# Kernel optimization log

Hardware: AMD Instinct MI355X
Metric: run time of the kernel (lower is better)

The kernel has to match this reference:

```python
import jax, jax.numpy as jnp
import numpy as np

B, N, E = 128, 300, 300        # batch, nodes (max_length), edges per sample
DIN, DH, DOUT = 768, 256, 256  # input feat, gcn hidden, gcn output
R = 26                         # NUM_DEP_TYPES
NHEADS, HDIM = 8, DH // 8


def setup_inputs() -> dict:
    key = jax.random.key(0)
    ks = jax.random.split(key, 12)
    s = lambda d: 1.0 / np.sqrt(d)
    return {
        "node_features": jax.random.normal(ks[0], (B, N, DIN), jnp.float32),
        "src": jax.random.randint(ks[1], (B, E), 0, N, jnp.int32),
        "dst": jax.random.randint(ks[2], (B, E), 0, N, jnp.int32),
        "etype": jax.random.randint(ks[3], (B, E), 0, R, jnp.int32),
        "W_rel": jax.random.normal(ks[4], (R, DIN, DH), jnp.float32) * s(DIN),
        "W_loop": jax.random.normal(ks[5], (DIN, DH), jnp.float32) * s(DIN),
        "b_rel": jnp.zeros((DH,), jnp.float32),
        "in_proj_w": jax.random.normal(ks[6], (3 * DH, DH), jnp.float32) * s(DH),
        "in_proj_b": jnp.zeros((3 * DH,), jnp.float32),
        "out_proj_w": jax.random.normal(ks[7], (DH, DH), jnp.float32) * s(DH),
        "out_proj_b": jnp.zeros((DH,), jnp.float32),
        "mlp_w": jax.random.normal(ks[8], (DOUT, DH), jnp.float32) * s(DH),
        "mlp_b": jnp.zeros((DOUT,), jnp.float32),
    }


def reference(node_features, src, dst, etype, W_rel, W_loop, b_rel,
              in_proj_w, in_proj_b, out_proj_w, out_proj_b, mlp_w, mlp_b):
    # ---- RelGraphConv (regularizer=None, self_loop=True, sum aggregation) ----
    # gather source-node features per edge: [B, E, DIN]
    h_src = jnp.take_along_axis(node_features, src[..., None].astype(jnp.int32), axis=1)
    # per-relation masked matmul: msg[b,e] = h_src[b,e] @ W_rel[etype[b,e]]
    msg = jnp.zeros((B, E, DH), node_features.dtype)
    for r in range(R):  # fixed small relation set
        mask = (etype == r)[..., None]
        msg = msg + jnp.einsum('bei,io->beo', jnp.where(mask, h_src, 0.0), W_rel[r])
    # scatter-add messages to destination nodes
    b_idx = jnp.arange(B)[:, None]
    agg = jnp.zeros((B, N, DH), node_features.dtype).at[b_idx, dst].add(msg)
    h = agg + jnp.einsum('bni,io->bno', node_features, W_loop) + b_rel  # [B, N, DH]

    # ---- MultiheadAttention (self-attn over nodes, eval mode) ----
    qkv = jnp.einsum('bnd,ed->bne', h, in_proj_w) + in_proj_b
    q, k, v = jnp.split(qkv, 3, axis=-1)
    q = q.reshape(B, N, NHEADS, HDIM)
    k = k.reshape(B, N, NHEADS, HDIM)
    v = v.reshape(B, N, NHEADS, HDIM)
    scores = jnp.einsum('bqhd,bkhd->bhqk', q, k) / np.sqrt(HDIM)
    attn = jax.nn.softmax(scores, axis=-1)
    ctx = jnp.einsum('bhqk,bkhd->bqhd', attn, v).reshape(B, N, DH)
    attn_out = jnp.einsum('bnd,ed->bne', ctx, out_proj_w) + out_proj_b

    # ---- mean-pool over nodes + MLP ----
    pooled = jnp.mean(attn_out, axis=1)  # [B, DH]
    return pooled @ mlp_w.T + mlp_b      # [B, DOUT]
```

## Files before the change

kernel.cpp:

```cpp
#include <hip/hip_runtime.h>
#include <hip/hip_bf16.h>
#include <cstdint>
#include <cstddef>

#define BB 128
#define NN 300
#define EE 300
#define DIN 768
#define DH 256
#define NREL 26
#define NHEADS 8
#define HDIM 32
#define MTOT (BB*NN)
#define NEDGE (BB*EE)
#define NHB 150

typedef __attribute__((ext_vector_type(8))) short bf16x8;
typedef __attribute__((ext_vector_type(4))) float f32x4;
typedef unsigned short u16;
union BU { uint4 u; bf16x8 v; };

__device__ __forceinline__ unsigned int packbf2(float a, float b) {
    unsigned int ua = __float_as_uint(a);
    unsigned int ub = __float_as_uint(b);
    ua = (ua + 0x7FFFu + ((ua >> 16) & 1u)) >> 16;
    ub = (ub + 0x7FFFu + ((ub >> 16) & 1u)) & 0xFFFF0000u;
    return ua | ub;
}
__device__ __forceinline__ u16 packbf1(float a) {
    unsigned int ua = __float_as_uint(a);
    return (u16)((ua + 0x7FFFu + ((ua >> 16) & 1u)) >> 16);
}
__device__ __forceinline__ unsigned cvtpk(float a, float b) {
    union { __hip_bfloat162 h; unsigned u; } cv;
    cv.h = __float22bfloat162_rn(make_float2(a, b));
    return cv.u;
}

__global__ __launch_bounds__(256) void b_hist(const int* __restrict__ etype,
                                              int* __restrict__ blockhist) {
    __shared__ int hist[NREL];
    const int tid = threadIdx.x;
    if (tid < NREL) hist[tid] = 0;
    __syncthreads();
    atomicAdd(&hist[etype[blockIdx.x * 256 + tid]], 1);
    __syncthreads();
    if (tid < NREL) blockhist[blockIdx.x * NREL + tid] = hist[tid];
}

__global__ __launch_bounds__(64) void b_scan(const int* __restrict__ blockhist,
                                             int* __restrict__ blockbase,
                                             int* __restrict__ cnt, int* __restrict__ off) {
    __shared__ int tot[NREL];
    const int r = threadIdx.x;
    if (r < NREL) {
        int run = 0;
        for (int b = 0; b < NHB; ++b) {
            blockbase[b * NREL + r] = run;
            run += blockhist[b * NREL + r];
        }
        tot[r] = run;
        cnt[r] = run;
    }
    __syncthreads();
    __shared__ int offs[NREL + 1];
    if (r == 0) {
        int acc = 0;
        for (int q = 0; q < NREL; ++q) { offs[q] = acc; off[q] = acc; acc += tot[q]; }
        offs[NREL] = acc; off[NREL] = acc;
    }
    __syncthreads();
    if (r < NREL) {
        int o = offs[r];
        for (int b = 0; b < NHB; ++b) blockbase[b * NREL + r] += o;
    }
}

__global__ __launch_bounds__(256) void b_scatter(const int* __restrict__ etype,
                                                 const int* __restrict__ blockbase,
                                                 int* __restrict__ list) {
    __shared__ int wavehist[4][NREL];
    __shared__ int waveoff[4][NREL];
    const int tid = threadIdx.x;
    const int w = tid >> 6, l = tid & 63;
    const int i = blockIdx.x * 256 + tid;
    const int r = etype[i];
    unsigned long long mymask = 0ull;
    #pragma unroll
    for (int q = 0; q < NREL; ++q) {
        unsigned long long m = __ballot(r == q);
        if (l == 0) wavehist[w][q] = __popcll(m);
        if (r == q) mymask = m;
    }
    const int myrank = __popcll(mymask & ((1ull << l) - 1ull));
    __syncthreads();
    if (tid < NREL) {
        int acc = 0;
        #pragma unroll
        for (int ww = 0; ww < 4; ++ww) { waveoff[ww][tid] = acc; acc += wavehist[ww][tid]; }
    }
    __syncthreads();
    list[blockbase[blockIdx.x * NREL + r] + waveoff[w][r] + myrank] = i;
}

__global__ __launch_bounds__(128) void z_tail(uint4* __restrict__ vg4) {
    const int p = blockIdx.x;
    const int tid = threadIdx.x;
    const int f = (tid < 64) ? 9 : 19;
    const int t = tid & 63;
    vg4[(size_t)(p * 20 + f) * 64 + t] = make_uint4(0u, 0u, 0u, 0u);
}

__global__ __launch_bounds__(256) void c_cast8(const float4* __restrict__ in,
                                               uint4* __restrict__ out, int n8) {
    int i = blockIdx.x * 256 + threadIdx.x;
    if (i < n8) {
        float4 f0 = in[2*i], f1 = in[2*i+1];
        uint4 o;
        o.x = packbf2(f0.x, f0.y); o.y = packbf2(f0.z, f0.w);
        o.z = packbf2(f1.x, f1.y); o.w = packbf2(f1.z, f1.w);
        out[i] = o;
    }
}

__global__ __launch_bounds__(256) void c_cast_w(
    const float* __restrict__ wrel, const float* __restrict__ wl, const float* __restrict__ wq,
    uint4* __restrict__ wrb, uint4* __restrict__ wlb, uint4* __restrict__ wqb) {
    int t = blockIdx.x * 256 + threadIdx.x;
    int l = t & 63, fid = t >> 6;
    if (fid < NREL*24*16) {
        int r = fid / 384, rem = fid - r * 384;
        int kf = rem >> 4, nt = rem & 15;
        int k0 = 32*kf + 8*(l >> 4), n = 16*nt + (l & 15);
        const float* p = wrel + ((size_t)r*768 + k0) * 256 + n;
        uint4 o;
        o.x = packbf2(p[0], p[256]); o.y = packbf2(p[512], p[768]);
        o.z = packbf2(p[1024], p[1280]); o.w = packbf2(p[1536], p[1792]);
        wrb[t] = o;
    } else if (fid < NREL*24*16 + 384) {
        int f2 = fid - NREL*24*16;
        int kf = f2 >> 4, nt = f2 & 15;
        int k0 = 32*kf + 8*(l >> 4), n = 16*nt + (l & 15);
        const float* p = wl + (size_t)k0 * 256 + n;
        uint4 o;
        o.x = packbf2(p[0], p[256]); o.y = packbf2(p[512], p[768]);
        o.z = packbf2(p[1024], p[1280]); o.w = packbf2(p[1536], p[1792]);
        wlb[f2*64 + l] = o;
    } else {
        int f2 = fid - NREL*24*16 - 384;
        int kf = f2 / 48, nt = f2 % 48;
        int e = 16*nt + (l & 15), d0 = 32*kf + 8*(l >> 4);
        const float4* p = (const float4*)(wq + (size_t)e * 256 + d0);
        float4 f0 = p[0], f1 = p[1];
        uint4 o;
        o.x = packbf2(f0.x, f0.y); o.y = packbf2(f0.z, f0.w);
        o.z = packbf2(f1.x, f1.y); o.w = packbf2(f1.z, f1.w);
        wqb[f2*64 + l] = o;
    }
}

__global__ __launch_bounds__(256) void k1m(
    const uint4* __restrict__ xb, const uint4* __restrict__ wlb,
    const float* __restrict__ brel, float* __restrict__ h) {
    __shared__ uint4 As[512];
    const int tid = threadIdx.x;
    const int m0 = blockIdx.x * 64;
    const int nb = blockIdx.y;
    const int w = tid >> 6, l = tid & 63;
    const int g = l >> 4, q = l & 15;
    int cA[2];
    #pragma unroll
    for (int p = 0; p < 2; ++p) {
        int s = tid + p * 256;
        int fi = s >> 6, l2 = s & 63;
        int kf = fi >> 2, mt = fi & 3;
        int row = m0 + 16*mt + (l2 & 15);
        cA[p] = row * 96 + 4*kf + (l2 >> 4);
    }
    f32x4 acc[4][2];
    #pragma unroll
    for (int a = 0; a < 4; ++a)
        #pragma unroll
        for (int n = 0; n < 2; ++n) acc[a][n] = (f32x4){0.f,0.f,0.f,0.f};

    for (int step = 0; step < 12; ++step) {
        uint4 a0 = xb[cA[0] + step*8];
        uint4 a1 = xb[cA[1] + step*8];
        BU Bf[2][2];
        #pragma unroll
        for (int kf = 0; kf < 2; ++kf)
            #pragma unroll
            for (int nt = 0; nt < 2; ++nt)
                Bf[kf][nt].u = wlb[((step*2 + kf)*16 + nb*8 + w*2 + nt)*64 + l];
        __syncthreads();
        As[tid] = a0; As[tid + 256] = a1;
        __syncthreads();
        #pragma unroll
        for (int kf = 0; kf < 2; ++kf) {
            BU Af[4];
            #pragma unroll
            for (int mt = 0; mt < 4; ++mt) Af[mt].u = As[(kf*4 + mt)*64 + l];
            #pragma unroll
            for (int mt = 0; mt < 4; ++mt)
                #pragma unroll
                for (int nt = 0; nt < 2; ++nt)
                    acc[mt][nt] = __builtin_amdgcn_mfma_f32_16x16x32_bf16(Af[mt].v, Bf[kf][nt].v, acc[mt][nt], 0, 0, 0);
        }
    }
    #pragma unroll
    for (int nt = 0; nt < 2; ++nt) {
        int col = nb*128 + w*32 + nt*16 + q;
        float bias = brel[col];
        #pragma unroll
        for (int mt = 0; mt < 4; ++mt)
            #pragma unroll
            for (int i = 0; i < 4; ++i)
                h[(size_t)(m0 + 16*mt + 4*g + i)*256 + col] = acc[mt][nt][i] + bias;
    }
}

__global__ __launch_bounds__(256) void k2m(
    const uint4* __restrict__ xb, const uint4* __restrict__ wrb,
    const int* __restrict__ src, const int* __restrict__ dst,
    const int* __restrict__ cnt, const int* __restrict__ off,
    const int* __restrict__ list, float* __restrict__ h) {
    __shared__ uint4 As[512];
    __shared__ int arow_s[64];
    __shared__ int drow_s[64];
    const int r = blockIdx.y;
    const int c_total = cnt[r];
    const int t0 = blockIdx.x * 64;
    if (t0 >= c_total) return;
    const int nb = blockIdx.z;
    const int tid = threadIdx.x;
    if (tid < 64) {
        int e = t0 + tid;
        int ar = 0, dr = -1;
        if (e < c_total) {
            int eid = list[off[r] + e];
            int b = eid / EE;
            ar = b * NN + src[eid];
            dr = b * NN + dst[eid];
        }
        arow_s[tid] = ar; drow_s[tid] = dr;
    }
    __syncthreads();
    const int w = tid >> 6, l = tid & 63;
    const int g = l >> 4, q = l & 15;
    int cA[2];
    #pragma unroll
    for (int p = 0; p < 2; ++p) {
        int s = tid + p * 256;
        int fi = s >> 6, l2 = s & 63;
        int kf = fi >> 2, mt = fi & 3;
        int row = arow_s[16*mt + (l2 & 15)];
        cA[p] = row * 96 + 4*kf + (l2 >> 4);
    }
    const uint4* wb = wrb + (size_t)r * 24*16*64;
    f32x4 acc[4][2];
    #pragma unroll
    for (int a = 0; a < 4; ++a)
        #pragma unroll
        for (int n = 0; n < 2; ++n) acc[a][n] = (f32x4){0.f,0.f,0.f,0.f};

    for (int step = 0; step < 12; ++step) {
        uint4 a0 = xb[cA[0] + step*8];
        uint4 a1 = xb[cA[1] + step*8];
        BU Bf[2][2];
        #pragma unroll
        for (int kf = 0; kf < 2; ++kf)
            #pragma unroll
            for (int nt = 0; nt < 2; ++nt)
                Bf[kf][nt].u = wb[((step*2 + kf)*16 + nb*8 + w*2 + nt)*64 + l];
        __syncthreads();
        As[tid] = a0; As[tid + 256] = a1;
        __syncthreads();
        #pragma unroll
        for (int kf = 0; kf < 2; ++kf) {
            BU Af[4];
            #pragma unroll
            for (int mt = 0; mt < 4; ++mt) Af[mt].u = As[(kf*4 + mt)*64 + l];
            #pragma unroll
            for (int mt = 0; mt < 4; ++mt)
                #pragma unroll
                for (int nt = 0; nt < 2; ++nt)
                    acc[mt][nt] = __builtin_amdgcn_mfma_f32_16x16x32_bf16(Af[mt].v, Bf[kf][nt].v, acc[mt][nt], 0, 0, 0);
        }
    }
    #pragma unroll
    for (int mt = 0; mt < 4; ++mt)
        #pragma unroll
        for (int i = 0; i < 4; ++i) {
            int dr = drow_s[16*mt + 4*g + i];
            if (dr >= 0) {
                #pragma unroll
                for (int nt = 0; nt < 2; ++nt)
                    atomicAdd(&h[(size_t)dr*256 + nb*128 + w*32 + nt*16 + q], acc[mt][nt][i]);
            }
        }
}

__global__ __launch_bounds__(256) void k3m(
    const uint4* __restrict__ hb, const uint4* __restrict__ wqb,
    const float* __restrict__ bq,
    u16* __restrict__ qg, u16* __restrict__ kg, u16* __restrict__ vg) {
    __shared__ uint4 As[512];
    const int tid = threadIdx.x;
    const int m0 = blockIdx.x * 64;
    const int nb = blockIdx.y;
    const int w = tid >> 6, l = tid & 63;
    const int g = l >> 4, q = l & 15;
    int cA[2];
    #pragma unroll
    for (int p = 0; p < 2; ++p) {
        int s = tid + p * 256;
        int fi = s >> 6, l2 = s & 63;
        int kf = fi >> 2, mt = fi & 3;
        int row = m0 + 16*mt + (l2 & 15);
        cA[p] = row * 32 + 4*kf + (l2 >> 4);
    }
    f32x4 acc[4][2];
    #pragma unroll
    for (int a = 0; a < 4; ++a)
        #pragma unroll
        for (int n = 0; n < 2; ++n) acc[a][n] = (f32x4){0.f,0.f,0.f,0.f};

    for (int step = 0; step < 4; ++step) {
        uint4 a0 = hb[cA[0] + step*8];
        uint4 a1 = hb[cA[1] + step*8];
        BU Bf[2][2];
        #pragma unroll
        for (int kf = 0; kf < 2; ++kf)
            #pragma unroll
            for (int nt = 0; nt < 2; ++nt)
                Bf[kf][nt].u = wqb[((step*2 + kf)*48 + nb*8 + w*2 + nt)*64 + l];
        __syncthreads();
        As[tid] = a0; As[tid + 256] = a1;
        __syncthreads();
        #pragma unroll
        for (int kf = 0; kf < 2; ++kf) {
            BU Af[4];
            #pragma unroll
            for (int mt = 0; mt < 4; ++mt) Af[mt].u = As[(kf*4 + mt)*64 + l];
            #pragma unroll
            for (int mt = 0; mt < 4; ++mt)
                #pragma unroll
                for (int nt = 0; nt < 2; ++nt)
                    acc[mt][nt] = __builtin_amdgcn_mfma_f32_16x16x32_bf16(Af[mt].v, Bf[kf][nt].v, acc[mt][nt], 0, 0, 0);
        }
    }
    #pragma unroll
    for (int nt = 0; nt < 2; ++nt) {
        int e = nb*128 + w*32 + nt*16 + q;
        float bias = bq[e];
        int region = e >> 8;
        int hh = (e & 255) >> 5;
        int d  = e & 31;
        u16* outb = (region == 0) ? qg : (region == 1) ? kg : vg;
        #pragma unroll
        for (int mt = 0; mt < 4; ++mt) {
            #pragma unroll
            for (int i = 0; i < 4; ++i) {
                int j = m0 + 16*mt + 4*g + i;
                int b_ = j / 300;
                int jn = j - b_ * 300;
                u16 val = packbf1(acc[mt][nt][i] + bias);
                size_t byte;
                if (region < 2) {
                    int word = ((b_*8 + hh)*19 + (jn >> 4))*64 + 16*(d >> 3) + (jn & 15);
                    byte = (size_t)word*16 + (size_t)(d & 7)*2;
                } else {
                    int word = ((b_*8 + hh)*20 + (d >> 4)*10 + (jn >> 5))*64 + 16*((jn >> 3) & 3) + (d & 15);
                    byte = (size_t)word*16 + (size_t)(jn & 7)*2;
                }
                *(u16*)((char*)outb + byte) = val;
            }
        }
    }
}

__global__ __launch_bounds__(256) void k4_attn(
    const uint4* __restrict__ qg, const uint4* __restrict__ kg,
    const uint4* __restrict__ vg, float* __restrict__ pooled) {
    __shared__ uint4 kf_s[19*64];
    __shared__ uint4 vt_s[20*64];
    __shared__ __align__(16) u16 pbuf[4][2560];
    __shared__ float pool_lds[4][32];
    const int bh = blockIdx.x;
    const int tid = threadIdx.x;
    for (int s = tid; s < 19*64; s += 256) kf_s[s] = kg[(size_t)bh*19*64 + s];
    for (int s = tid; s < 20*64; s += 256) vt_s[s] = vg[(size_t)bh*20*64 + s];
    __syncthreads();

    const int w = tid >> 6, l = tid & 63;
    const int g = l >> 4, q = l & 15;
    char* pwbase = (char*)pbuf[w] + 256*(g >> 1) + 16*q + 8*(g & 1);
    const uint4* prd = (const uint4*)pbuf[w];

    const float c1 = 0.17677669529663687f * 1.4426950408889634f;
    float pool[8] = {0.f,0.f,0.f,0.f,0.f,0.f,0.f,0.f};

    for (int qt = w; qt < 19; qt += 4) {
        const int qrow = qt * 16 + q;
        BU uq; uq.u = qg[(size_t)(bh*19 + qt)*64 + l];
        float lsum = 0.f;
        f32x4 ctx0 = {0.f,0.f,0.f,0.f}, ctx1 = {0.f,0.f,0.f,0.f};

        #pragma unroll
        for (int half = 0; half < 2; ++half) {
            #pragma unroll
            for (int jj = 0; jj < 10; ++jj) {
                const int jt = half*10 + jj;
                uint2 pk = make_uint2(0u, 0u);
                if (jt < 19) {
                    BU uk; uk.u = kf_s[jt*64 + l];
                    f32x4 z = {0.f,0.f,0.f,0.f};
                    f32x4 s4 = __builtin_amdgcn_mfma_f32_16x16x32_bf16(uk.v, uq.v, z, 0, 0, 0);
                    float p0 = exp2f(s4[0]*c1);
                    float p1 = exp2f(s4[1]*c1);
                    float p2 = exp2f(s4[2]*c1);
                    float p3 = exp2f(s4[3]*c1);
                    if (jt == 18 && g == 3) { p0 = 0.f; p1 = 0.f; p2 = 0.f; p3 = 0.f; }
                    lsum += (p0 + p1) + (p2 + p3);
                    pk.x = cvtpk(p0, p1);
                    pk.y = cvtpk(p2, p3);
                }
                *(uint2*)(pwbase + 512*jj) = pk;
            }
            #pragma unroll
            for (int cc = 0; cc < 5; ++cc) {
                const int cg = half*5 + cc;
                BU up;  up.u  = prd[cc*64 + l];
                BU uv0; uv0.u = vt_s[cg*64 + l];
                BU uv1; uv1.u = vt_s[(10 + cg)*64 + l];
                ctx0 = __builtin_amdgcn_mfma_f32_16x16x32_bf16(uv0.v, up.v, ctx0, 0, 0, 0);
                ctx1 = __builtin_amdgcn_mfma_f32_16x16x32_bf16(uv1.v, up.v, ctx1, 0, 0, 0);
            }
        }
        lsum += __shfl_xor(lsum, 16);
        lsum += __shfl_xor(lsum, 32);
        if (qrow < NN) {
            float inv = 1.0f / lsum;
            pool[0] += ctx0[0] * inv; pool[1] += ctx0[1] * inv;
            pool[2] += ctx0[2] * inv; pool[3] += ctx0[3] * inv;
            pool[4] += ctx1[0] * inv; pool[5] += ctx1[1] * inv;
            pool[6] += ctx1[2] * inv; pool[7] += ctx1[3] * inv;
        }
    }

    #pragma unroll
    for (int i = 0; i < 8; ++i) {
        float v = pool[i];
        v += __shfl_xor(v, 1); v += __shfl_xor(v, 2);
        v += __shfl_xor(v, 4); v += __shfl_xor(v, 8);
        pool[i] = v;
    }
    if (q == 0) {
        #pragma unroll
        for (int dt = 0; dt < 2; ++dt)
            #pragma unroll
            for (int i = 0; i < 4; ++i)
                pool_lds[w][dt * 16 + 4 * g + i] = pool[dt * 4 + i];
    }
    __syncthreads();
    if (tid < 32) {
        int b = bh >> 3, hh = bh & 7;
        float s = pool_lds[0][tid] + pool_lds[1][tid] + pool_lds[2][tid] + pool_lds[3][tid];
        pooled[(size_t)b * DH + hh * HDIM + tid] = s * (1.0f / 300.0f);
    }
}

__global__ __launch_bounds__(256) void k5_head(
    const float* __restrict__ pooled, const float* __restrict__ wo, const float* __restrict__ bo,
    const float* __restrict__ wm, const float* __restrict__ bm, float* __restrict__ out) {
    __shared__ float pc[DH];
    __shared__ float t1[DH];
    const int b = blockIdx.x, tid = threadIdx.x;
    pc[tid] = pooled[(size_t)b * DH + tid];
    __syncthreads();
    float acc = bo[tid];
    for (int d = 0; d < DH; ++d) acc += pc[d] * wo[(size_t)tid * DH + d];
    t1[tid] = acc;
    __syncthreads();
    float acc2 = bm[tid];
    for (int e2 = 0; e2 < DH; ++e2) acc2 += t1[e2] * wm[(size_t)tid * DH + e2];
    out[(size_t)b * DH + tid] = acc2;
}

extern "C" void kernel_launch(void* const* d_in, const int* in_sizes, int n_in,
                              void* d_out, int out_size, void* d_ws, size_t ws_size,
                              hipStream_t stream) {
    (void)in_sizes; (void)n_in; (void)out_size; (void)ws_size;
    const float* x     = (const float*)d_in[0];
    const int*   src   = (const int*)d_in[1];
    const int*   dst   = (const int*)d_in[2];
    const int*   etype = (const int*)d_in[3];
    const float* wrel  = (const float*)d_in[4];
    const float* wloop = (const float*)d_in[5];
    const float* brel  = (const float*)d_in[6];
    const float* wq    = (const float*)d_in[7];
    const float* bq    = (const float*)d_in[8];
    const float* wo    = (const float*)d_in[9];
    const float* bo    = (const float*)d_in[10];
    const float* wm    = (const float*)d_in[11];
    const float* bm    = (const float*)d_in[12];
    float* out = (float*)d_out;

    char* W = (char*)d_ws;
    float* h      = (float*)W;
    u16*   vg     = (u16*)W;
    u16*   xb     = (u16*)(W + 39321600ull);
    u16*   qg     = xb;
    u16*   kg     = (u16*)(W + 39321600ull + 19922944ull);
    u16*   hb     = (u16*)(W + 39321600ull + 58982400ull);
    uint4* wrb    = (uint4*)(W + 39321600ull + 58982400ull + 19660800ull);
    uint4* wlb    = (uint4*)((char*)wrb + 10223616ull);
    uint4* wqb    = (uint4*)((char*)wlb + 393216ull);
    float* pooled = (float*)((char*)wqb + 393216ull);
    int*   ibase  = (int*)((char*)pooled + 131072ull);
    int*   cnt    = ibase;
    int*   off    = ibase + 32;
    int*   list   = ibase + 64;
    int*   blockhist = list + NEDGE;
    int*   blockbase = blockhist + NHB*NREL;

    b_hist<<<NHB, 256, 0, stream>>>(etype, blockhist);
    b_scan<<<1, 64, 0, stream>>>(blockhist, blockbase, cnt, off);
    b_scatter<<<NHB, 256, 0, stream>>>(etype, blockbase, list);

    c_cast8<<<14400, 256, 0, stream>>>((const float4*)x, (uint4*)xb, 3686400);
    c_cast_w<<<2688, 256, 0, stream>>>(wrel, wloop, wq, wrb, wlb, wqb);

    k1m<<<dim3(600, 2), 256, 0, stream>>>((const uint4*)xb, wlb, brel, h);
    k2m<<<dim3(32, 26, 2), 256, 0, stream>>>((const uint4*)xb, wrb, src, dst, cnt, off, list, h);
    c_cast8<<<4800, 256, 0, stream>>>((const float4*)h, (uint4*)hb, 1228800);
    z_tail<<<1024, 128, 0, stream>>>((uint4*)vg);
    k3m<<<dim3(600, 6), 256, 0, stream>>>((const uint4*)hb, wqb, bq, qg, kg, vg);
    k4_attn<<<BB * NHEADS, 256, 0, stream>>>((const uint4*)qg, (const uint4*)kg, (const uint4*)vg, pooled);
    k5_head<<<BB, 256, 0, stream>>>(pooled, wo, bo, wm, bm, out);
}
```

Baseline: 268.8 us.

## Fuse h bf16 cast into QKV GEMM and enlarge row tiles in graph-conv GEMMs

The separate cast of the fp32 hidden state to bf16 is removed. k3m now reads fp32 h directly, converts its 64-row tile into LDS once, and loops over all six output column blocks, so each A tile is reused instead of being reloaded per column block. k1m and k2m move from 64-row to 128-row tiles, which halves weight-fragment reloads per row but doubles accumulator registers and LDS use. Because h is now read while q/k/v are written, the v buffer is moved out of h's aliased region into a later part of the workspace. This relies on the workspace being large enough.

```diff
diff --git a/kernel.cpp b/kernel.cpp
--- a/kernel.cpp
+++ b/kernel.cpp
@@ -162,30 +162,32 @@
 __global__ __launch_bounds__(256) void k1m(
     const uint4* __restrict__ xb, const uint4* __restrict__ wlb,
     const float* __restrict__ brel, float* __restrict__ h) {
-    __shared__ uint4 As[512];
-    const int tid = threadIdx.x;
-    const int m0 = blockIdx.x * 64;
+    __shared__ uint4 As[1024];
+    const int tid = threadIdx.x;
+    const int m0 = blockIdx.x * 128;
     const int nb = blockIdx.y;
     const int w = tid >> 6, l = tid & 63;
     const int g = l >> 4, q = l & 15;
-    int cA[2];
-    #pragma unroll
-    for (int p = 0; p < 2; ++p) {
+    int cA[4];
+    #pragma unroll
+    for (int p = 0; p < 4; ++p) {
         int s = tid + p * 256;
         int fi = s >> 6, l2 = s & 63;
-        int kf = fi >> 2, mt = fi & 3;
+        int kf = fi >> 3, mt = fi & 7;
         int row = m0 + 16*mt + (l2 & 15);
         cA[p] = row * 96 + 4*kf + (l2 >> 4);
     }
-    f32x4 acc[4][2];
-    #pragma unroll
-    for (int a = 0; a < 4; ++a)
+    f32x4 acc[8][2];
+    #pragma unroll
+    for (int a = 0; a < 8; ++a)
         #pragma unroll
         for (int n = 0; n < 2; ++n) acc[a][n] = (f32x4){0.f,0.f,0.f,0.f};
 
     for (int step = 0; step < 12; ++step) {
         uint4 a0 = xb[cA[0] + step*8];
         uint4 a1 = xb[cA[1] + step*8];
+        uint4 a2 = xb[cA[2] + step*8];
+        uint4 a3 = xb[cA[3] + step*8];
         BU Bf[2][2];
         #pragma unroll
         for (int kf = 0; kf < 2; ++kf)
@@ -193,18 +195,17 @@
             for (int nt = 0; nt < 2; ++nt)
                 Bf[kf][nt].u = wlb[((step*2 + kf)*16 + nb*8 + w*2 + nt)*64 + l];
         __syncthreads();
-        As[tid] = a0; As[tid + 256] = a1;
+        As[tid] = a0; As[tid + 256] = a1; As[tid + 512] = a2; As[tid + 768] = a3;
         __syncthreads();
         #pragma unroll
         for (int kf = 0; kf < 2; ++kf) {
-            BU Af[4];
-            #pragma unroll
-            for (int mt = 0; mt < 4; ++mt) Af[mt].u = As[(kf*4 + mt)*64 + l];
-            #pragma unroll
-            for (int mt = 0; mt < 4; ++mt)
+            #pragma unroll
+            for (int mt = 0; mt < 8; ++mt) {
+                BU Af; Af.u = As[(kf*8 + mt)*64 + l];
                 #pragma unroll
                 for (int nt = 0; nt < 2; ++nt)
-                    acc[mt][nt] = __builtin_amdgcn_mfma_f32_16x16x32_bf16(Af[mt].v, Bf[kf][nt].v, acc[mt][nt], 0, 0, 0);
+                    acc[mt][nt] = __builtin_amdgcn_mfma_f32_16x16x32_bf16(Af.v, Bf[kf][nt].v, acc[mt][nt], 0, 0, 0);
+            }
         }
     }
     #pragma unroll
@@ -212,7 +213,7 @@
         int col = nb*128 + w*32 + nt*16 + q;
         float bias = brel[col];
         #pragma unroll
-        for (int mt = 0; mt < 4; ++mt)
+        for (int mt = 0; mt < 8; ++mt)
             #pragma unroll
             for (int i = 0; i < 4; ++i)
                 h[(size_t)(m0 + 16*mt + 4*g + i)*256 + col] = acc[mt][nt][i] + bias;
@@ -224,16 +225,16 @@
     const int* __restrict__ src, const int* __restrict__ dst,
     const int* __restrict__ cnt, const int* __restrict__ off,
     const int* __restrict__ list, float* __restrict__ h) {
-    __shared__ uint4 As[512];
-    __shared__ int arow_s[64];
-    __shared__ int drow_s[64];
+    __shared__ uint4 As[1024];
+    __shared__ int arow_s[128];
+    __shared__ int drow_s[128];
     const int r = blockIdx.y;
     const int c_total = cnt[r];
-    const int t0 = blockIdx.x * 64;
+    const int t0 = blockIdx.x * 128;
     if (t0 >= c_total) return;
     const int nb = blockIdx.z;
     const int tid = threadIdx.x;
-    if (tid < 64) {
+    if (tid < 128) {
         int e = t0 + tid;
         int ar = 0, dr = -1;
         if (e < c_total) {
@@ -247,25 +248,27 @@
     __syncthreads();
     const int w = tid >> 6, l = tid & 63;
     const int g = l >> 4, q = l & 15;
-    int cA[2];
-    #pragma unroll
-    for (int p = 0; p < 2; ++p) {
+    int cA[4];
+    #pragma unroll
+    for (int p = 0; p < 4; ++p) {
         int s = tid + p * 256;
         int fi = s >> 6, l2 = s & 63;
-        int kf = fi >> 2, mt = fi & 3;
+        int kf = fi >> 3, mt = fi & 7;
         int row = arow_s[16*mt + (l2 & 15)];
         cA[p] = row * 96 + 4*kf + (l2 >> 4);
     }
     const uint4* wb = wrb + (size_t)r * 24*16*64;
-    f32x4 acc[4][2];
-    #pragma unroll
-    for (int a = 0; a < 4; ++a)
+    f32x4 acc[8][2];
+    #pragma unroll
+    for (int a = 0; a < 8; ++a)
         #pragma unroll
         for (int n = 0; n < 2; ++n) acc[a][n] = (f32x4){0.f,0.f,0.f,0.f};
 
     for (int step = 0; step < 12; ++step) {
         uint4 a0 = xb[cA[0] + step*8];
         uint4 a1 = xb[cA[1] + step*8];
+        uint4 a2 = xb[cA[2] + step*8];
+        uint4 a3 = xb[cA[3] + step*8];
         BU Bf[2][2];
         #pragma unroll
         for (int kf = 0; kf < 2; ++kf)
@@ -273,22 +276,21 @@
             for (int nt = 0; nt < 2; ++nt)
                 Bf[kf][nt].u = wb[((step*2 + kf)*16 + nb*8 + w*2 + nt)*64 + l];
         __syncthreads();
-        As[tid] = a0; As[tid + 256] = a1;
+        As[tid] = a0; As[tid + 256] = a1; As[tid + 512] = a2; As[tid + 768] = a3;
         __syncthreads();
         #pragma unroll
         for (int kf = 0; kf < 2; ++kf) {
-            BU Af[4];
-            #pragma unroll
-            for (int mt = 0; mt < 4; ++mt) Af[mt].u = As[(kf*4 + mt)*64 + l];
-            #pragma unroll
-            for (int mt = 0; mt < 4; ++mt)
+            #pragma unroll
+            for (int mt = 0; mt < 8; ++mt) {
+                BU Af; Af.u = As[(kf*8 + mt)*64 + l];
                 #pragma unroll
                 for (int nt = 0; nt < 2; ++nt)
-                    acc[mt][nt] = __builtin_amdgcn_mfma_f32_16x16x32_bf16(Af[mt].v, Bf[kf][nt].v, acc[mt][nt], 0, 0, 0);
-        }
-    }
-    #pragma unroll
-    for (int mt = 0; mt < 4; ++mt)
+                    acc[mt][nt] = __builtin_amdgcn_mfma_f32_16x16x32_bf16(Af.v, Bf[kf][nt].v, acc[mt][nt], 0, 0, 0);
+            }
+        }
+    }
+    #pragma unroll
+    for (int mt = 0; mt < 8; ++mt)
         #pragma unroll
         for (int i = 0; i < 4; ++i) {
             int dr = drow_s[16*mt + 4*g + i];
@@ -301,79 +303,83 @@
 }
 
 __global__ __launch_bounds__(256) void k3m(
-    const uint4* __restrict__ hb, const uint4* __restrict__ wqb,
+    const float* __restrict__ h, const uint4* __restrict__ wqb,
     const float* __restrict__ bq,
     u16* __restrict__ qg, u16* __restrict__ kg, u16* __restrict__ vg) {
-    __shared__ uint4 As[512];
+    __shared__ uint4 Aall[2048];
     const int tid = threadIdx.x;
     const int m0 = blockIdx.x * 64;
-    const int nb = blockIdx.y;
     const int w = tid >> 6, l = tid & 63;
     const int g = l >> 4, q = l & 15;
-    int cA[2];
-    #pragma unroll
-    for (int p = 0; p < 2; ++p) {
+
+    #pragma unroll
+    for (int p = 0; p < 8; ++p) {
         int s = tid + p * 256;
         int fi = s >> 6, l2 = s & 63;
         int kf = fi >> 2, mt = fi & 3;
         int row = m0 + 16*mt + (l2 & 15);
-        cA[p] = row * 32 + 4*kf + (l2 >> 4);
-    }
-    f32x4 acc[4][2];
-    #pragma unroll
-    for (int a = 0; a < 4; ++a)
-        #pragma unroll
-        for (int n = 0; n < 2; ++n) acc[a][n] = (f32x4){0.f,0.f,0.f,0.f};
-
-    for (int step = 0; step < 4; ++step) {
-        uint4 a0 = hb[cA[0] + step*8];
-        uint4 a1 = hb[cA[1] + step*8];
-        BU Bf[2][2];
-        #pragma unroll
-        for (int kf = 0; kf < 2; ++kf)
-            #pragma unroll
-            for (int nt = 0; nt < 2; ++nt)
-                Bf[kf][nt].u = wqb[((step*2 + kf)*48 + nb*8 + w*2 + nt)*64 + l];
-        __syncthreads();
-        As[tid] = a0; As[tid + 256] = a1;
-        __syncthreads();
-        #pragma unroll
-        for (int kf = 0; kf < 2; ++kf) {
-            BU Af[4];
-            #pragma unroll
-            for (int mt = 0; mt < 4; ++mt) Af[mt].u = As[(kf*4 + mt)*64 + l];
-            #pragma unroll
-            for (int mt = 0; mt < 4; ++mt)
+        int k0 = 32*kf + 8*(l2 >> 4);
+        const float4* hp = (const float4*)(h + (size_t)row * 256 + k0);
+        float4 f0 = hp[0], f1 = hp[1];
+        uint4 o;
+        o.x = packbf2(f0.x, f0.y); o.y = packbf2(f0.z, f0.w);
+        o.z = packbf2(f1.x, f1.y); o.w = packbf2(f1.z, f1.w);
+        Aall[s] = o;
+    }
+    __syncthreads();
+
+    for (int nb = 0; nb < 6; ++nb) {
+        f32x4 acc[4][2];
+        #pragma unroll
+        for (int a = 0; a < 4; ++a)
+            #pragma unroll
+            for (int n = 0; n < 2; ++n) acc[a][n] = (f32x4){0.f,0.f,0.f,0.f};
+
+        #pragma unroll
+        for (int step = 0; step < 4; ++step) {
+            BU Bf[2][2];
+            #pragma unroll
+            for (int kf = 0; kf < 2; ++kf)
                 #pragma unroll
                 for (int nt = 0; nt < 2; ++nt)
-                    acc[mt][nt] = __builtin_amdgcn_mfma_f32_16x16x32_bf16(Af[mt].v, Bf[kf][nt].v, acc[mt][nt], 0, 0, 0);
-        }
-    }
-    #pragma unroll
-    for (int nt = 0; nt < 2; ++nt) {
-        int e = nb*128 + w*32 + nt*16 + q;
-        float bias = bq[e];
-        int region = e >> 8;
-        int hh = (e & 255) >> 5;
-        int d  = e & 31;
-        u16* outb = (region == 0) ? qg : (region == 1) ? kg : vg;
-        #pragma unroll
-        for (int mt = 0; mt < 4; ++mt) {
-            #pragma unroll
-            for (int i = 0; i < 4; ++i) {
-                int j = m0 + 16*mt + 4*g + i;
-                int b_ = j / 300;
-                int jn = j - b_ * 300;
-                u16 val = packbf1(acc[mt][nt][i] + bias);
-                size_t byte;
-                if (region < 2) {
-                    int word = ((b_*8 + hh)*19 + (jn >> 4))*64 + 16*(d >> 3) + (jn & 15);
-                    byte = (size_t)word*16 + (size_t)(d & 7)*2;
-                } else {
-                    int word = ((b_*8 + hh)*20 + (d >> 4)*10 + (jn >> 5))*64 + 16*((jn >> 3) & 3) + (d & 15);
-                    byte = (size_t)word*16 + (size_t)(jn & 7)*2;
+                    Bf[kf][nt].u = wqb[((step*2 + kf)*48 + nb*8 + w*2 + nt)*64 + l];
+            #pragma unroll
+            for (int kf = 0; kf < 2; ++kf) {
+                #pragma unroll
+                for (int mt = 0; mt < 4; ++mt) {
+                    BU Af; Af.u = Aall[((step*2 + kf)*4 + mt)*64 + l];
+                    #pragma unroll
+                    for (int nt = 0; nt < 2; ++nt)
+                        acc[mt][nt] = __builtin_amdgcn_mfma_f32_16x16x32_bf16(Af.v, Bf[kf][nt].v, acc[mt][nt], 0, 0, 0);
                 }
-                *(u16*)((char*)outb + byte) = val;
+            }
+        }
+        #pragma unroll
+        for (int nt = 0; nt < 2; ++nt) {
+            int e = nb*128 + w*32 + nt*16 + q;
+            float bias = bq[e];
+            int region = e >> 8;
+            int hh = (e & 255) >> 5;
+            int d  = e & 31;
+            u16* outb = (region == 0) ? qg : (region == 1) ? kg : vg;
+            #pragma unroll
+            for (int mt = 0; mt < 4; ++mt) {
+                #pragma unroll
+                for (int i = 0; i < 4; ++i) {
+                    int j = m0 + 16*mt + 4*g + i;
+                    int b_ = j / 300;
+                    int jn = j - b_ * 300;
+                    u16 val = packbf1(acc[mt][nt][i] + bias);
+                    size_t byte;
+                    if (region < 2) {
+                        int word = ((b_*8 + hh)*19 + (jn >> 4))*64 + 16*(d >> 3) + (jn & 15);
+                        byte = (size_t)word*16 + (size_t)(d & 7)*2;
+                    } else {
+                        int word = ((b_*8 + hh)*20 + (d >> 4)*10 + (jn >> 5))*64 + 16*((jn >> 3) & 3) + (d & 15);
+                        byte = (size_t)word*16 + (size_t)(jn & 7)*2;
+                    }
+                    *(u16*)((char*)outb + byte) = val;
+                }
             }
         }
     }
@@ -512,7 +518,7 @@
     u16*   xb     = (u16*)(W + 39321600ull);
     u16*   qg     = xb;
     u16*   kg     = (u16*)(W + 39321600ull + 19922944ull);
-    u16*   hb     = (u16*)(W + 39321600ull + 58982400ull);
+    u16*   hb_dead= (u16*)(W + 39321600ull + 58982400ull);
     uint4* wrb    = (uint4*)(W + 39321600ull + 58982400ull + 19660800ull);
     uint4* wlb    = (uint4*)((char*)wrb + 10223616ull);
     uint4* wqb    = (uint4*)((char*)wlb + 393216ull);
@@ -523,6 +529,10 @@
     int*   list   = ibase + 64;
     int*   blockhist = list + NEDGE;
     int*   blockbase = blockhist + NHB*NREL;
+    (void)hb_dead;
+
+    vg = (u16*)((char*)(blockbase + NHB*NREL) + 256);
+    vg = (u16*)(((uintptr_t)vg + 255) & ~(uintptr_t)255);
 
     b_hist<<<NHB, 256, 0, stream>>>(etype, blockhist);
     b_scan<<<1, 64, 0, stream>>>(blockhist, blockbase, cnt, off);
@@ -531,11 +541,10 @@
     c_cast8<<<14400, 256, 0, stream>>>((const float4*)x, (uint4*)xb, 3686400);
     c_cast_w<<<2688, 256, 0, stream>>>(wrel, wloop, wq, wrb, wlb, wqb);
 
-    k1m<<<dim3(600, 2), 256, 0, stream>>>((const uint4*)xb, wlb, brel, h);
-    k2m<<<dim3(32, 26, 2), 256, 0, stream>>>((const uint4*)xb, wrb, src, dst, cnt, off, list, h);
-    c_cast8<<<4800, 256, 0, stream>>>((const float4*)h, (uint4*)hb, 1228800);
+    k1m<<<dim3(300, 2), 256, 0, stream>>>((const uint4*)xb, wlb, brel, h);
+    k2m<<<dim3(16, 26, 2), 256, 0, stream>>>((const uint4*)xb, wrb, src, dst, cnt, off, list, h);
     z_tail<<<1024, 128, 0, stream>>>((uint4*)vg);
-    k3m<<<dim3(600, 6), 256, 0, stream>>>((const uint4*)hb, wqb, bq, qg, kg, vg);
+    k3m<<<600, 256, 0, stream>>>(h, wqb, bq, qg, kg, vg);
     k4_attn<<<BB * NHEADS, 256, 0, stream>>>((const uint4*)qg, (const uint4*)kg, (const uint4*)vg, pooled);
     k5_head<<<BB, 256, 0, stream>>>(pooled, wo, bo, wm, bm, out);
 }
```

New measurement: 285.0 us. 1.06x slower.
